# Kernel tuning notes

Measured on AMD Instinct MI355X. Metric: run time of the kernel, lower is better.

The kernel has to match this reference:

```python
import jax, jax.numpy as jnp
import numpy as np

EMBED_DIM = 2048
NUM_CODEBOOKS = 256          # C
CODES_PER_CODEBOOK = 4096    # K
CODEBOOK_DIM = EMBED_DIM // NUM_CODEBOOKS  # d = 8 (also dim_memory)


def setup_inputs() -> dict:
    key = jax.random.key(0)
    k_x, k_keys, k_vals = jax.random.split(key, 3)
    embeddings = jax.random.normal(k_x, (8, EMBED_DIM, 4, 4), dtype=jnp.float32)
    # VQ codebook keys (one codebook per head) and learned memory values
    keys = jax.random.normal(k_keys, (NUM_CODEBOOKS, CODES_PER_CODEBOOK, CODEBOOK_DIM), dtype=jnp.float32)
    values = jax.random.normal(k_vals, (NUM_CODEBOOKS, CODES_PER_CODEBOOK, CODEBOOK_DIM), dtype=jnp.float32)
    return {"embeddings": embeddings, "keys": keys, "values": values}


def reference(embeddings, keys, values):
    # embeddings: [B, D, H, W] -> tokens [B, N, D] (N = H*W), as in the torch wrapper
    B, D, H, W = embeddings.shape
    C, K, d = keys.shape  # num_codebooks, codes_per_codebook, codebook_dim
    N = H * W
    x = embeddings.reshape(B, D, N).transpose(0, 2, 1)      # [B, N, D]
    x = x.reshape(B, N, C, d)                               # split into per-codebook heads

    # Euclidean nearest-code search per codebook (eval mode: no EMA update)
    dots = jnp.einsum('bncd,ckd->bnck', x, keys)            # [B, N, C, K]
    dist = (jnp.sum(x * x, axis=-1)[..., None]
            - 2.0 * dots
            + jnp.sum(keys * keys, axis=-1)[None, None, :, :])
    idx = jnp.argmin(dist, axis=-1)                         # [B, N, C] int indices

    # Gather memory values: values[c, idx[b,n,c]] -> [B, N, C, d]
    mem = values[jnp.arange(C)[None, None, :], idx]

    # concat heads, then undo the wrapper's permute/reshape
    out = mem.reshape(B, N, C * d).transpose(0, 2, 1).reshape(B, D, H, W)
    return out
```

## Files before the change

kernel.cpp:

```cpp
#include <hip/hip_runtime.h>

#define C_NUM   256
#define K_CODES 4096
#define D_CB    8
#define THREADS 512
#define WAVES   8
#define TPW     16
#define CHUNKS  (K_CODES / 64)

__global__ __launch_bounds__(THREADS, 2)
void dkvb_kernel(const float* __restrict__ emb,
                 const float* __restrict__ keys,
                 const float* __restrict__ values,
                 float* __restrict__ out) {
    __shared__ float xs[128][D_CB];

    const int c    = blockIdx.x;
    const int tid  = threadIdx.x;
    const int wave = tid >> 6;
    const int lane = tid & 63;

    {
        int e = tid;
        #pragma unroll
        for (int r = 0; r < 2; ++r, e += THREADS) {
            const int t = e >> 3, j = e & 7;
            xs[t][j] = emb[(size_t)(t >> 4) * 32768 + c * 128 + j * 16 + (t & 15)];
        }
    }
    __syncthreads();

    float x[TPW][8];
    float x2[TPW];
    #pragma unroll
    for (int t = 0; t < TPW; ++t) {
        #pragma unroll
        for (int j = 0; j < 8; ++j) x[t][j] = xs[wave * TPW + t][j];
        float s = x[t][0] * x[t][0];
        #pragma unroll
        for (int j = 1; j < 8; ++j) s = fmaf(x[t][j], x[t][j], s);
        x2[t] = s;
    }

    float bestd[TPW];
    int   besti[TPW];
    #pragma unroll
    for (int t = 0; t < TPW; ++t) { bestd[t] = 3.4028235e38f; besti[t] = 0; }

    const float4* kb = (const float4*)(keys + (size_t)c * K_CODES * D_CB);
    float4 a0 = kb[lane * 2];
    float4 a1 = kb[lane * 2 + 1];
    for (int ch = 0; ch < CHUNKS; ++ch) {
        const int nc = (ch + 1 < CHUNKS) ? (ch + 1) : ch;
        const float4 b0 = kb[nc * 128 + lane * 2];
        const float4 b1 = kb[nc * 128 + lane * 2 + 1];

        const int code = ch * 64 + lane;
        float k2 = a0.x * a0.x;
        k2 = fmaf(a0.y, a0.y, k2);
        k2 = fmaf(a0.z, a0.z, k2);
        k2 = fmaf(a0.w, a0.w, k2);
        k2 = fmaf(a1.x, a1.x, k2);
        k2 = fmaf(a1.y, a1.y, k2);
        k2 = fmaf(a1.z, a1.z, k2);
        k2 = fmaf(a1.w, a1.w, k2);

        #pragma unroll
        for (int t = 0; t < TPW; ++t) {
            float d = x[t][0] * a0.x;
            d = fmaf(x[t][1], a0.y, d);
            d = fmaf(x[t][2], a0.z, d);
            d = fmaf(x[t][3], a0.w, d);
            d = fmaf(x[t][4], a1.x, d);
            d = fmaf(x[t][5], a1.y, d);
            d = fmaf(x[t][6], a1.z, d);
            d = fmaf(x[t][7], a1.w, d);
            const float dist = fmaf(d, -2.0f, x2[t] + k2);
            const bool lt = dist < bestd[t];
            bestd[t] = lt ? dist : bestd[t];
            besti[t] = lt ? code : besti[t];
        }
        a0 = b0; a1 = b1;
    }

    int myidx = 0;
    #pragma unroll
    for (int t = 0; t < TPW; ++t) {
        float d = bestd[t];
        int   i = besti[t];
        #pragma unroll
        for (int m = 32; m >= 1; m >>= 1) {
            const float od = __shfl_xor(d, m, 64);
            const int   oi = __shfl_xor(i, m, 64);
            if (od < d || (od == d && oi < i)) { d = od; i = oi; }
        }
        if (lane == t) myidx = i;
    }

    if (lane < TPW) {
        const int tg = wave * TPW + lane;
        const int b = tg >> 4, n = tg & 15;
        const float4* vr = (const float4*)(values + ((size_t)c * K_CODES + myidx) * D_CB);
        const float4 v0 = vr[0];
        const float4 v1 = vr[1];
        float* op = out + (size_t)b * 32768 + c * 128 + n;
        op[0]   = v0.x; op[16]  = v0.y; op[32]  = v0.z; op[48]  = v0.w;
        op[64]  = v1.x; op[80]  = v1.y; op[96]  = v1.z; op[112] = v1.w;
    }
}

extern "C" void kernel_launch(void* const* d_in, const int* in_sizes, int n_in,
                              void* d_out, int out_size, void* d_ws, size_t ws_size,
                              hipStream_t stream) {
    const float* emb    = (const float*)d_in[0];
    const float* keys   = (const float*)d_in[1];
    const float* values = (const float*)d_in[2];
    float* out = (float*)d_out;
    dkvb_kernel<<<C_NUM, THREADS, 0, stream>>>(emb, keys, values, out);
}
```

Before: 50.33 us.

## Compute VQ distances with bf16 split-precision MFMA and exact fp32 rescoring

Replaces the scalar fp32 distance loop with MFMA 16x16x32 bf16 matrix ops. Each operand is split into hi/lo bf16 pairs, and the norm terms are folded into the matrix product. Keys are staged in shared memory per 1024-code chunk, and a packed key (truncated distance | index) tracks the top-2 candidates. Tokens whose top-2 gap falls below a fixed margin are recomputed exactly in fp32 over all codes. The risk is wrong indices when approximation error exceeds the margin, plus extra overhead from the rescoring path.

```diff
diff --git a/kernel.cpp b/kernel.cpp
--- a/kernel.cpp
+++ b/kernel.cpp
@@ -1,109 +1,217 @@
 #include <hip/hip_runtime.h>
 
-#define C_NUM   256
-#define K_CODES 4096
-#define D_CB    8
-#define THREADS 512
-#define WAVES   8
-#define TPW     16
-#define CHUNKS  (K_CODES / 64)
+#define C_NUM    256
+#define KCODES   4096
+#define THREADS  512
+#define CHUNK    1024
+#define NCHUNK   4
+#define NTILES   (CHUNK / 16)
+#define AROW     80
+#define MARGIN   0.125f
+
+#define OFF_A    0
+#define OFF_XS   (CHUNK * AROW)
+#define OFF_BEST (OFF_XS + 4096)
+#define OFF_UL   (OFF_BEST + 512)
+#define OFF_NU   (OFF_UL + 512)
+#define SMEM_SZ  (OFF_NU + 16)
+
+typedef short  bf16x8 __attribute__((ext_vector_type(8)));
+typedef float  f32x4  __attribute__((ext_vector_type(4)));
+typedef float  v4f    __attribute__((ext_vector_type(4)));
+
+__device__ __forceinline__ unsigned short bf16rn(float f) {
+    unsigned u = __float_as_uint(f);
+    u += 0x7FFFu + ((u >> 16) & 1u);
+    return (unsigned short)(u >> 16);
+}
+__device__ __forceinline__ float bf16tof(unsigned short h) {
+    return __uint_as_float(((unsigned)h) << 16);
+}
 
 __global__ __launch_bounds__(THREADS, 2)
 void dkvb_kernel(const float* __restrict__ emb,
                  const float* __restrict__ keys,
                  const float* __restrict__ values,
                  float* __restrict__ out) {
-    __shared__ float xs[128][D_CB];
+    extern __shared__ unsigned char sm[];
+    float (*xs)[8] = (float(*)[8])(sm + OFF_XS);
+    int* best  = (int*)(sm + OFF_BEST);
+    int* ulist = (int*)(sm + OFF_UL);
+    int* nu    = (int*)(sm + OFF_NU);
 
     const int c    = blockIdx.x;
     const int tid  = threadIdx.x;
     const int wave = tid >> 6;
     const int lane = tid & 63;
-
+    const int col  = lane & 15;
+    const int g    = lane >> 4;
+    const int arow = lane & 15;
+
+    const v4f* kb4 = (const v4f*)(keys + (size_t)c * KCODES * 8);
+
+    if (tid == 0) *nu = 0;
+
+    #pragma unroll
+    for (int r = 0; r < 2; ++r) {
+        const int e = tid + r * THREADS;
+        const int t = e >> 3, j = e & 7;
+        xs[t][j] = emb[(size_t)(t >> 4) * 32768 + c * 128 + j * 16 + (t & 15)];
+    }
+    __syncthreads();
+
+    bf16x8 bfrag;
     {
-        int e = tid;
-        #pragma unroll
-        for (int r = 0; r < 2; ++r, e += THREADS) {
-            const int t = e >> 3, j = e & 7;
-            xs[t][j] = emb[(size_t)(t >> 4) * 32768 + c * 128 + j * 16 + (t & 15)];
+        const int t = wave * 16 + col;
+        float xv[8];
+        #pragma unroll
+        for (int j = 0; j < 8; ++j) xv[j] = xs[t][j];
+        float x2 = xv[0] * xv[0];
+        #pragma unroll
+        for (int j = 1; j < 8; ++j) x2 = fmaf(xv[j], xv[j], x2);
+        bf16x8 fxh, fxl, fct;
+        #pragma unroll
+        for (int j = 0; j < 8; ++j) {
+            const unsigned short h = bf16rn(xv[j]);
+            fxh[j] = (short)h;
+            fxl[j] = (short)bf16rn(xv[j] - bf16tof(h));
+        }
+        const unsigned short x2h = bf16rn(x2);
+        const unsigned short x2l = bf16rn(x2 - bf16tof(x2h));
+        fct[0] = (short)0x3F80; fct[1] = (short)0x3F80;
+        fct[2] = (short)x2h;    fct[3] = (short)x2l;
+        fct[4] = 0; fct[5] = 0; fct[6] = 0; fct[7] = 0;
+        bfrag = (g < 2) ? fxh : ((g == 2) ? fxl : fct);
+    }
+
+    const f32x4 zeroC = {0.f, 0.f, 0.f, 0.f};
+    unsigned m1 = 0xFFFFFFFFu, m2 = 0xFFFFFFFFu;
+    const int rowbase = g * 4;
+
+    for (int ph = 0; ph < NCHUNK; ++ph) {
+        const int cbase = ph * CHUNK;
+
+        #pragma unroll
+        for (int r = 0; r < 2; ++r) {
+            const int ci   = r * THREADS + tid;
+            const int code = cbase + ci;
+            const v4f p0 = kb4[code * 2];
+            const v4f p1 = kb4[code * 2 + 1];
+            float kk[8] = {p0.x, p0.y, p0.z, p0.w, p1.x, p1.y, p1.z, p1.w};
+            float k2 = kk[0] * kk[0];
+            #pragma unroll
+            for (int j = 1; j < 8; ++j) k2 = fmaf(kk[j], kk[j], k2);
+            unsigned short th[8], tl[8];
+            #pragma unroll
+            for (int j = 0; j < 8; ++j) {
+                const float tt = -2.0f * kk[j];
+                th[j] = bf16rn(tt);
+                tl[j] = bf16rn(tt - bf16tof(th[j]));
+            }
+            const unsigned short k2h = bf16rn(k2);
+            const unsigned short k2l = bf16rn(k2 - bf16tof(k2h));
+            unsigned w[16];
+            #pragma unroll
+            for (int i = 0; i < 4; ++i) w[i]     = (unsigned)th[2*i] | ((unsigned)th[2*i+1] << 16);
+            #pragma unroll
+            for (int i = 0; i < 4; ++i) w[4 + i] = (unsigned)tl[2*i] | ((unsigned)tl[2*i+1] << 16);
+            #pragma unroll
+            for (int i = 0; i < 4; ++i) w[8 + i] = w[i];
+            w[12] = (unsigned)k2h | ((unsigned)k2l << 16);
+            w[13] = 0x3F803F80u;
+            w[14] = 0u; w[15] = 0u;
+            uint4* dst = (uint4*)(sm + OFF_A + (size_t)ci * AROW);
+            dst[0] = make_uint4(w[0],  w[1],  w[2],  w[3]);
+            dst[1] = make_uint4(w[4],  w[5],  w[6],  w[7]);
+            dst[2] = make_uint4(w[8],  w[9],  w[10], w[11]);
+            dst[3] = make_uint4(w[12], w[13], w[14], w[15]);
+        }
+        __syncthreads();
+
+        const unsigned char* abase = sm + OFF_A + (size_t)arow * AROW + (size_t)g * 16;
+        for (int tile = 0; tile < NTILES; ++tile) {
+            const bf16x8 afrag = *(const bf16x8*)(abase + tile * (16 * AROW));
+            const f32x4 D = __builtin_amdgcn_mfma_f32_16x16x32_bf16(afrag, bfrag, zeroC, 0, 0, 0);
+            const int codeb = cbase + tile * 16 + rowbase;
+            #pragma unroll
+            for (int r2 = 0; r2 < 4; ++r2) {
+                const unsigned key = (__float_as_uint(D[r2]) & 0xFFFFF000u) | (unsigned)(codeb + r2);
+                const unsigned hi = (m1 > key) ? m1 : key;
+                m1 = (m1 < key) ? m1 : key;
+                m2 = (m2 < hi) ? m2 : hi;
+            }
+        }
+        __syncthreads();
+    }
+
+    #pragma unroll
+    for (int sh = 16; sh <= 32; sh <<= 1) {
+        const unsigned o1 = (unsigned)__shfl_xor((int)m1, sh, 64);
+        const unsigned o2 = (unsigned)__shfl_xor((int)m2, sh, 64);
+        const unsigned hi  = (m1 > o1) ? m1 : o1;
+        m1 = (m1 < o1) ? m1 : o1;
+        const unsigned mn2 = (m2 < o2) ? m2 : o2;
+        m2 = (mn2 < hi) ? mn2 : hi;
+    }
+    if (lane < 16) {
+        const int t = wave * 16 + lane;
+        best[t] = (int)(m1 & 0xFFFu);
+        const float v1 = __uint_as_float(m1 & 0xFFFFF000u);
+        const float v2 = __uint_as_float(m2 & 0xFFFFF000u);
+        if (v2 - v1 < MARGIN) {
+            const int idx = atomicAdd(nu, 1);
+            ulist[idx] = t;
         }
     }
     __syncthreads();
 
-    float x[TPW][8];
-    float x2[TPW];
-    #pragma unroll
-    for (int t = 0; t < TPW; ++t) {
-        #pragma unroll
-        for (int j = 0; j < 8; ++j) x[t][j] = xs[wave * TPW + t][j];
-        float s = x[t][0] * x[t][0];
-        #pragma unroll
-        for (int j = 1; j < 8; ++j) s = fmaf(x[t][j], x[t][j], s);
-        x2[t] = s;
-    }
-
-    float bestd[TPW];
-    int   besti[TPW];
-    #pragma unroll
-    for (int t = 0; t < TPW; ++t) { bestd[t] = 3.4028235e38f; besti[t] = 0; }
-
-    const float4* kb = (const float4*)(keys + (size_t)c * K_CODES * D_CB);
-    float4 a0 = kb[lane * 2];
-    float4 a1 = kb[lane * 2 + 1];
-    for (int ch = 0; ch < CHUNKS; ++ch) {
-        const int nc = (ch + 1 < CHUNKS) ? (ch + 1) : ch;
-        const float4 b0 = kb[nc * 128 + lane * 2];
-        const float4 b1 = kb[nc * 128 + lane * 2 + 1];
-
-        const int code = ch * 64 + lane;
-        float k2 = a0.x * a0.x;
-        k2 = fmaf(a0.y, a0.y, k2);
-        k2 = fmaf(a0.z, a0.z, k2);
-        k2 = fmaf(a0.w, a0.w, k2);
-        k2 = fmaf(a1.x, a1.x, k2);
-        k2 = fmaf(a1.y, a1.y, k2);
-        k2 = fmaf(a1.z, a1.z, k2);
-        k2 = fmaf(a1.w, a1.w, k2);
-
-        #pragma unroll
-        for (int t = 0; t < TPW; ++t) {
-            float d = x[t][0] * a0.x;
-            d = fmaf(x[t][1], a0.y, d);
-            d = fmaf(x[t][2], a0.z, d);
-            d = fmaf(x[t][3], a0.w, d);
-            d = fmaf(x[t][4], a1.x, d);
-            d = fmaf(x[t][5], a1.y, d);
-            d = fmaf(x[t][6], a1.z, d);
-            d = fmaf(x[t][7], a1.w, d);
-            const float dist = fmaf(d, -2.0f, x2[t] + k2);
-            const bool lt = dist < bestd[t];
-            bestd[t] = lt ? dist : bestd[t];
-            besti[t] = lt ? code : besti[t];
-        }
-        a0 = b0; a1 = b1;
-    }
-
-    int myidx = 0;
-    #pragma unroll
-    for (int t = 0; t < TPW; ++t) {
-        float d = bestd[t];
-        int   i = besti[t];
-        #pragma unroll
-        for (int m = 32; m >= 1; m >>= 1) {
-            const float od = __shfl_xor(d, m, 64);
-            const int   oi = __shfl_xor(i, m, 64);
-            if (od < d || (od == d && oi < i)) { d = od; i = oi; }
-        }
-        if (lane == t) myidx = i;
-    }
-
-    if (lane < TPW) {
-        const int tg = wave * TPW + lane;
-        const int b = tg >> 4, n = tg & 15;
-        const float4* vr = (const float4*)(values + ((size_t)c * K_CODES + myidx) * D_CB);
-        const float4 v0 = vr[0];
-        const float4 v1 = vr[1];
-        float* op = out + (size_t)b * 32768 + c * 128 + n;
+    const int NU = *nu;
+    for (int e = wave; e < NU; e += 8) {
+        const int t = ulist[e];
+        float xp[8];
+        #pragma unroll
+        for (int j = 0; j < 8; ++j) xp[j] = -2.0f * xs[t][j];
+        float bd = 3.4028235e38f;
+        int   bi = 0;
+        for (int it = 0; it < 64; ++it) {
+            const int code = it * 64 + lane;
+            const v4f p0 = kb4[code * 2];
+            const v4f p1 = kb4[code * 2 + 1];
+            float k2 = p0.x * p0.x;
+            k2 = fmaf(p0.y, p0.y, k2);
+            k2 = fmaf(p0.z, p0.z, k2);
+            k2 = fmaf(p0.w, p0.w, k2);
+            k2 = fmaf(p1.x, p1.x, k2);
+            k2 = fmaf(p1.y, p1.y, k2);
+            k2 = fmaf(p1.z, p1.z, k2);
+            k2 = fmaf(p1.w, p1.w, k2);
+            float d = fmaf(xp[0], p0.x, k2);
+            d = fmaf(xp[1], p0.y, d);
+            d = fmaf(xp[2], p0.z, d);
+            d = fmaf(xp[3], p0.w, d);
+            d = fmaf(xp[4], p1.x, d);
+            d = fmaf(xp[5], p1.y, d);
+            d = fmaf(xp[6], p1.z, d);
+            d = fmaf(xp[7], p1.w, d);
+            if (d < bd) { bd = d; bi = code; }
+        }
+        #pragma unroll
+        for (int msk = 32; msk >= 1; msk >>= 1) {
+            const float od = __shfl_xor(bd, msk, 64);
+            const int   oi = __shfl_xor(bi, msk, 64);
+            if (od < bd || (od == bd && oi < bi)) { bd = od; bi = oi; }
+        }
+        if (lane == 0) best[t] = bi;
+    }
+    __syncthreads();
+
+    if (tid < 128) {
+        const int t = tid;
+        const int code = best[t];
+        const v4f* vr = (const v4f*)(values + ((size_t)c * KCODES + code) * 8);
+        const v4f v0 = vr[0];
+        const v4f v1 = vr[1];
+        float* op = out + (size_t)(t >> 4) * 32768 + c * 128 + (t & 15);
         op[0]   = v0.x; op[16]  = v0.y; op[32]  = v0.z; op[48]  = v0.w;
         op[64]  = v1.x; op[80]  = v1.y; op[96]  = v1.z; op[112] = v1.w;
     }
@@ -116,5 +224,8 @@
     const float* keys   = (const float*)d_in[1];
     const float* values = (const float*)d_in[2];
     float* out = (float*)d_out;
-    dkvb_kernel<<<C_NUM, THREADS, 0, stream>>>(emb, keys, values, out);
-}
+
+    hipFuncSetAttribute((const void*)dkvb_kernel,
+                        hipFuncAttributeMaxDynamicSharedMemorySize, SMEM_SZ);
+    dkvb_kernel<<<C_NUM, THREADS, SMEM_SZ, stream>>>(emb, keys, values, out);
+}
```

Measured after the change: 80.56 us. 1.6x slower.
